# Optimization experiments

Hardware: AMD Instinct MI355X
Metric: run time of the kernel (lower is better)

Reference implementation:

```python
import jax, jax.numpy as jnp
import numpy as np

EPS = 1e-4  # BatchNorm2d eps from source


def binarize(x):
    # brevitas 1-bit quant: sign(x) with sign(0)=+1; straight-through (clipped) estimator
    y = jnp.clip(x, -1.0, 1.0)
    q = jnp.where(x >= 0, 1.0, -1.0).astype(x.dtype)
    return y + jax.lax.stop_gradient(q - y)


def bn(x, g, b, m, v):
    inv = g / jnp.sqrt(v + EPS)
    return x * inv[None, :, None, None] + (b - m * inv)[None, :, None, None]


def conv(x, w, pad):
    return jax.lax.conv_general_dilated(
        x, w, window_strides=(1, 1), padding=[(pad, pad), (pad, pad)],
        dimension_numbers=('NCHW', 'OIHW', 'NCHW'))


def conv_mod(x, w1, bn1, w3, bn3):
    # conv1x1(binary W) -> BN -> binarize act -> conv3x3(binary W) -> BN -> binarize act
    x = conv(x, binarize(w1), 0)
    x = binarize(bn(x, *bn1))
    x = conv(x, binarize(w3), 1)
    x = binarize(bn(x, *bn3))
    return x


def maxpool2(x):
    return jax.lax.reduce_window(x, -jnp.inf, jax.lax.max,
                                 (1, 1, 2, 2), (1, 1, 2, 2), 'VALID')


def setup_inputs() -> dict:
    key = jax.random.key(0)
    ks = jax.random.split(key, 24)
    B, Cin, down, up, H, W = 16, 256, 64, 256, 56, 56
    d = {
        'x':   jax.random.normal(ks[0], (B, Cin, H, W), jnp.float32),
        'w11': jax.random.normal(ks[1], (down, Cin, 1, 1), jnp.float32) * 0.1,
        'w31': jax.random.normal(ks[2], (up, down, 3, 3), jnp.float32) * 0.1,
        'w12': jax.random.normal(ks[3], (down, up, 1, 1), jnp.float32) * 0.1,
        'w32': jax.random.normal(ks[4], (up, down, 3, 3), jnp.float32) * 0.1,
    }
    # BatchNorm params (inference stats): gamma, beta, running mean, running var
    for i, (tag, c) in enumerate([('11', down), ('31', up), ('12', down), ('32', up)]):
        d['g' + tag] = jax.random.uniform(ks[5 + 4 * i], (c,), jnp.float32, 0.5, 1.5)
        d['b' + tag] = jax.random.normal(ks[6 + 4 * i], (c,), jnp.float32) * 0.1
        d['m' + tag] = jax.random.normal(ks[7 + 4 * i], (c,), jnp.float32) * 0.1
        d['v' + tag] = jax.random.uniform(ks[8 + 4 * i], (c,), jnp.float32, 0.5, 1.5)
    return d


def reference(x, w11, w31, w12, w32,
              g11, b11, m11, v11, g31, b31, m31, v31,
              g12, b12, m12, v12, g32, b32, m32, v32):
    h = conv_mod(x, w11, (g11, b11, m11, v11), w31, (g31, b31, m31, v31))
    r = conv_mod(h, w12, (g12, b12, m12, v12), w32, (g32, b32, m32, v32))
    s = binarize(h + r)          # quant_add: re-binarize the residual sum
    return maxpool2(s)           # MaxPool2d(2)
```

## Files before the change

### kernel.cpp

```cpp
#include <hip/hip_runtime.h>
#include <stdint.h>

#pragma clang fp contract(off)


#define HW_   3136
#define NPIX  50176

#define OFF_W31B   0
#define OFF_W12B   18432
#define OFF_W32B   20480
#define OFF_IV11   38912
#define OFF_IV31   39424
#define OFF_IV12   41472
#define OFF_IV32   41984
#define OFF_SGNT   44032
#define OFF_A1     109568
#define OFF_A2     510976
#define OFF_H      912384
#define OFF_S      2518016

__device__ inline float2 mk_ivbt(float g, float b, float m, float v) {
    float inv  = __fdiv_rn(g, __fsqrt_rn(__fadd_rn(v, 1e-4f)));
    float beta = __fsub_rn(b, __fmul_rn(m, inv));
    return make_float2(inv, beta);
}

__global__ __launch_bounds__(256) void k0_all(
    const float* __restrict__ w11, const float* __restrict__ w31,
    const float* __restrict__ w12, const float* __restrict__ w32,
    const float* __restrict__ g11, const float* __restrict__ b11,
    const float* __restrict__ m11, const float* __restrict__ v11,
    const float* __restrict__ g31, const float* __restrict__ b31,
    const float* __restrict__ m31, const float* __restrict__ v31,
    const float* __restrict__ g12, const float* __restrict__ b12,
    const float* __restrict__ m12, const float* __restrict__ v12,
    const float* __restrict__ g32, const float* __restrict__ b32,
    const float* __restrict__ m32, const float* __restrict__ v32,
    uint64_t* __restrict__ W31b, uint64_t* __restrict__ W12b,
    uint64_t* __restrict__ W32b,
    float2* __restrict__ iv11, float2* __restrict__ iv31,
    float2* __restrict__ iv12, float2* __restrict__ iv32,
    float* __restrict__ sgnT)
{
    int blk = blockIdx.x;
    if (blk < 1216) {
        int wid = blk * 4 + (threadIdx.x >> 6);
        int l = threadIdx.x & 63;
        if (wid < 2304) {
            int co = wid / 9, tap = wid % 9;
            uint64_t bits = __ballot(w31[(co * 64 + l) * 9 + tap] >= 0.f);
            if (l == 0) W31b[wid] = bits;
        } else if (wid < 4608) {
            int i = wid - 2304;
            int co = i / 9, tap = i % 9;
            uint64_t bits = __ballot(w32[(co * 64 + l) * 9 + tap] >= 0.f);
            if (l == 0) W32b[i] = bits;
        } else if (wid < 4864) {
            int i = wid - 4608;
            int co = i >> 2, k = i & 3;
            uint64_t bits = __ballot(w12[co * 256 + k * 64 + l] >= 0.f);
            if (l == 0) W12b[i] = bits;
        }
    } else if (blk < 1219) {
        int i = (blk - 1216) * 256 + threadIdx.x;
        if (i < 64)        iv11[i]       = mk_ivbt(g11[i],       b11[i],       m11[i],       v11[i]);
        else if (i < 320)  iv31[i - 64]  = mk_ivbt(g31[i - 64],  b31[i - 64],  m31[i - 64],  v31[i - 64]);
        else if (i < 384)  iv12[i - 320] = mk_ivbt(g12[i - 320], b12[i - 320], m12[i - 320], v12[i - 320]);
        else if (i < 640)  iv32[i - 384] = mk_ivbt(g32[i - 384], b32[i - 384], m32[i - 384], v32[i - 384]);
    } else {
        int t = (blk - 1219) * 256 + threadIdx.x;
        int j = t >> 8, ci = t & 255;
        sgnT[ci * 64 + j] = (w11[t] >= 0.f) ? 1.0f : -1.0f;
    }
}

__global__ __launch_bounds__(512) void k1_conv1(
    const float* __restrict__ x, const float* __restrict__ sgnT,
    const float2* __restrict__ ivbt, unsigned char* __restrict__ A1)
{
    __shared__ float sgn[16384];

#pragma unroll
    for (int i = 0; i < 32; ++i)
        sgn[i * 512 + threadIdx.x] = sgnT[i * 512 + threadIdx.x];

    const int l = threadIdx.x & 63;
    const int g = __builtin_amdgcn_readfirstlane(threadIdx.x >> 6);
    const int P = blockIdx.x * 128 + l * 2;
    const int bl = P / HW_;
    const int pxl = P - bl * HW_;
    const float* xp = x + (size_t)bl * (256 * HW_) + pxl;
    const float* sg = sgn + g * 8;

    float acc[8][2];
#pragma unroll
    for (int j = 0; j < 8; ++j) { acc[j][0] = 0.0f; acc[j][1] = 0.0f; }

    float2 b0[8], b1[8], b2[8], b3[8];

#define PF(B, CI0)                                                          \
    _Pragma("unroll")                                                       \
    for (int k = 0; k < 8; ++k)                                             \
        B[k] = *(const float2*)(xp + (size_t)((CI0) + k) * HW_);

#define COMP(B, CI0)                                                        \
    _Pragma("unroll")                                                       \
    for (int k = 0; k < 8; ++k) {                                           \
        const float* s_ = sg + ((CI0) + k) * 64;                            \
        _Pragma("unroll")                                                   \
        for (int j = 0; j < 8; ++j) {                                       \
            acc[j][0] = __builtin_fmaf(s_[j], B[k].x, acc[j][0]);           \
            acc[j][1] = __builtin_fmaf(s_[j], B[k].y, acc[j][1]);           \
        }                                                                   \
    }

    PF(b0, 0) PF(b1, 8) PF(b2, 16)

    __syncthreads();

    for (int cb = 0; cb < 256; cb += 32) {
        PF(b3, cb + 24) COMP(b0, cb)
        if (cb < 224) {
            PF(b0, cb + 32) COMP(b1, cb + 8)
            PF(b1, cb + 40) COMP(b2, cb + 16)
            PF(b2, cb + 48) COMP(b3, cb + 24)
        } else {
            COMP(b1, 232) COMP(b2, 240) COMP(b3, 248)
        }
    }
#undef PF
#undef COMP

    unsigned bp0 = 0, bp1 = 0;
#pragma unroll
    for (int j = 0; j < 8; ++j) {
        float2 ib = ivbt[g * 8 + j];
        bp0 |= (__fadd_rn(__fmul_rn(acc[j][0], ib.x), ib.y) >= 0.0f) ? (1u << j) : 0u;
        bp1 |= (__fadd_rn(__fmul_rn(acc[j][1], ib.x), ib.y) >= 0.0f) ? (1u << j) : 0u;
    }
    unsigned char* a = A1 + (size_t)P * 8 + g;
    a[0] = (unsigned char)bp0;
    a[8] = (unsigned char)bp1;
}

template <bool MERGE>
__global__ __launch_bounds__(256) void k_conv3b(
    const uint64_t* __restrict__ A, const uint64_t* __restrict__ Wb,
    const float2* __restrict__ ivbt, const uint64_t* __restrict__ Hin,
    uint64_t* __restrict__ Out)
{
    __shared__ uint64_t tile[4 * 58];
    const int l = threadIdx.x & 63;
    const int wv = threadIdx.x >> 6;
    const int chunk = blockIdx.x;
    const int b = chunk / 49;
    const int hw0 = (chunk % 49) * 64;
    const int r0 = hw0 / 56;
    const int o  = hw0 % 56;
    const int rfirst = r0 - 1;

    {
        int idx = threadIdx.x;
        if (idx < 4 * 58) {
            int rr = idx / 58, cc = idx % 58;
            int gh = rfirst + rr, gw = cc - 1;
            uint64_t v = 0;
            if ((unsigned)gh < 56u && (unsigned)gw < 56u)
                v = A[b * HW_ + gh * 56 + gw];
            tile[idx] = v;
        }
    }

    const int co = wv * 64 + l;
    uint64_t wp[9];
    int c64[9];
#pragma unroll
    for (int t = 0; t < 9; ++t) {
        wp[t] = Wb[co * 9 + t];
        c64[t] = 64 - 2 * (int)__popcll(wp[t]);
    }
    const float2 ib = ivbt[co];

    __syncthreads();

    uint64_t res = 0;
    for (int p = 0; p < 64; ++p) {
        const int inrow2 = (p >= 56 - o) ? 1 : 0;
        const int w = o + p - (inrow2 ? 56 : 0);
        const int row = r0 + inrow2;
        const int rbase = inrow2 * 58;

        int s = 0;
#pragma unroll
        for (int dr = 0; dr < 3; ++dr)
#pragma unroll
            for (int dc = 0; dc < 3; ++dc) {
                uint64_t a = tile[rbase + dr * 58 + w + dc];
                s += (int)__popcll(a ^ wp[dr * 3 + dc]);
            }
        int y = 576 - 2 * s;

        unsigned um = 0;
        if (row == 0)  um |= 0x007u;
        if (row == 55) um |= 0x1C0u;
        if (w == 0)    um |= 0x049u;
        if (w == 55)   um |= 0x124u;
        if (um) {
#pragma unroll
            for (int t = 0; t < 9; ++t)
                if ((um >> t) & 1u) y -= c64[t];
        }

        float val = __fadd_rn(__fmul_rn((float)y, ib.x), ib.y);
        uint64_t word = __ballot(val >= 0.0f);
        res = (l == p) ? word : res;
    }

    size_t oidx = (size_t)wv * NPIX + (size_t)(b * HW_) + hw0 + l;
    if (MERGE) res |= Hin[oidx];
    Out[oidx] = res;
}

__global__ __launch_bounds__(256) void k3_conv1b(
    const uint64_t* __restrict__ H, const uint64_t* __restrict__ W12b,
    const float2* __restrict__ ivbt, uint64_t* __restrict__ A2)
{
    int p = blockIdx.x * 256 + threadIdx.x;
    uint64_t h0 = H[p];
    uint64_t h1 = H[NPIX + p];
    uint64_t h2 = H[2 * NPIX + p];
    uint64_t h3 = H[3 * NPIX + p];
    uint64_t bits = 0;
#pragma unroll 4
    for (int co = 0; co < 64; ++co) {
        const uint64_t* wp = W12b + co * 4;
        int s = (int)(__popcll(h0 ^ wp[0]) + __popcll(h1 ^ wp[1]) +
                      __popcll(h2 ^ wp[2]) + __popcll(h3 ^ wp[3]));
        int y = 256 - 2 * s;
        float2 ib = ivbt[co];
        float val = __fadd_rn(__fmul_rn((float)y, ib.x), ib.y);
        bits |= (uint64_t)(val >= 0.0f) << co;
    }
    A2[p] = bits;
}

__global__ __launch_bounds__(256) void k4b_pool(
    const uint64_t* __restrict__ S, float* __restrict__ out)
{
    int o = blockIdx.x * 256 + threadIdx.x;
    int ow = o % 28;
    int t = o / 28;
    int oh = t % 28; t /= 28;
    int co = t & 255;
    int b  = t >> 8;
    int k = co >> 6, j = co & 63;
    const uint64_t* Sk = S + (size_t)k * NPIX + (size_t)(b * HW_) + (2 * oh) * 56 + 2 * ow;
    uint64_t s = Sk[0] | Sk[1] | Sk[56] | Sk[57];
    out[o] = ((s >> j) & 1) ? 1.0f : -1.0f;
}

extern "C" void kernel_launch(void* const* d_in, const int* in_sizes, int n_in,
                              void* d_out, int out_size, void* d_ws, size_t ws_size,
                              hipStream_t stream)
{
    const float* x   = (const float*)d_in[0];
    const float* w11 = (const float*)d_in[1];
    const float* w31 = (const float*)d_in[2];
    const float* w12 = (const float*)d_in[3];
    const float* w32 = (const float*)d_in[4];
    const float* g11 = (const float*)d_in[5];
    const float* b11 = (const float*)d_in[6];
    const float* m11 = (const float*)d_in[7];
    const float* v11 = (const float*)d_in[8];
    const float* g31 = (const float*)d_in[9];
    const float* b31 = (const float*)d_in[10];
    const float* m31 = (const float*)d_in[11];
    const float* v31 = (const float*)d_in[12];
    const float* g12 = (const float*)d_in[13];
    const float* b12 = (const float*)d_in[14];
    const float* m12 = (const float*)d_in[15];
    const float* v12 = (const float*)d_in[16];
    const float* g32 = (const float*)d_in[17];
    const float* b32 = (const float*)d_in[18];
    const float* m32 = (const float*)d_in[19];
    const float* v32 = (const float*)d_in[20];

    char* ws = (char*)d_ws;
    uint64_t* W31b = (uint64_t*)(ws + OFF_W31B);
    uint64_t* W12b = (uint64_t*)(ws + OFF_W12B);
    uint64_t* W32b = (uint64_t*)(ws + OFF_W32B);
    float2* iv11 = (float2*)(ws + OFF_IV11);
    float2* iv31 = (float2*)(ws + OFF_IV31);
    float2* iv12 = (float2*)(ws + OFF_IV12);
    float2* iv32 = (float2*)(ws + OFF_IV32);
    float*  sgnT = (float*)(ws + OFF_SGNT);
    uint64_t* A1 = (uint64_t*)(ws + OFF_A1);
    uint64_t* A2 = (uint64_t*)(ws + OFF_A2);
    uint64_t* Hb = (uint64_t*)(ws + OFF_H);
    uint64_t* Sb = (uint64_t*)(ws + OFF_S);

    k0_all<<<dim3(1283), dim3(256), 0, stream>>>(
        w11, w31, w12, w32,
        g11, b11, m11, v11, g31, b31, m31, v31,
        g12, b12, m12, v12, g32, b32, m32, v32,
        W31b, W12b, W32b, iv11, iv31, iv12, iv32, sgnT);

    k1_conv1<<<dim3(392), dim3(512), 0, stream>>>(x, sgnT, iv11, (unsigned char*)A1);

    k_conv3b<false><<<dim3(784), dim3(256), 0, stream>>>(A1, W31b, iv31, (const uint64_t*)nullptr, Hb);

    k3_conv1b<<<dim3(196), dim3(256), 0, stream>>>(Hb, W12b, iv12, A2);

    k_conv3b<true><<<dim3(784), dim3(256), 0, stream>>>(A2, W32b, iv32, Hb, Sb);

    k4b_pool<<<dim3(12544), dim3(256), 0, stream>>>(Sb, (float*)d_out);
}
```

Baseline: 125.8 us.

## Fuse binary 1x1 conv into first 3x3 conv; drop LDS sign staging in conv1

The separate k3_conv1b kernel is folded into the first k_conv3b launch. Each block shares its freshly computed H words through LDS, and each wave computes 16 of the 64 output channels, writing 16-bit fragments of A2. This removes a launch and a global read of H. Separately, k1_conv1 no longer copies the sign matrix into LDS and reads it directly from global memory. Its prefetch pipeline shrinks from four buffers to two and adds per-iteration barriers, which may lower memory-level parallelism in that kernel.

```diff
diff --git a/kernel.cpp b/kernel.cpp
--- a/kernel.cpp
+++ b/kernel.cpp
@@ -79,25 +79,19 @@
     const float* __restrict__ x, const float* __restrict__ sgnT,
     const float2* __restrict__ ivbt, unsigned char* __restrict__ A1)
 {
-    __shared__ float sgn[16384];
-
-#pragma unroll
-    for (int i = 0; i < 32; ++i)
-        sgn[i * 512 + threadIdx.x] = sgnT[i * 512 + threadIdx.x];
-
     const int l = threadIdx.x & 63;
     const int g = __builtin_amdgcn_readfirstlane(threadIdx.x >> 6);
     const int P = blockIdx.x * 128 + l * 2;
     const int bl = P / HW_;
     const int pxl = P - bl * HW_;
     const float* xp = x + (size_t)bl * (256 * HW_) + pxl;
-    const float* sg = sgn + g * 8;
+    const float* sg = sgnT + g * 8;
 
     float acc[8][2];
 #pragma unroll
     for (int j = 0; j < 8; ++j) { acc[j][0] = 0.0f; acc[j][1] = 0.0f; }
 
-    float2 b0[8], b1[8], b2[8], b3[8];
+    float2 bufA[8], bufB[8];
 
 #define PF(B, CI0)                                                          \
     _Pragma("unroll")                                                       \
@@ -115,19 +109,14 @@
         }                                                                   \
     }
 
-    PF(b0, 0) PF(b1, 8) PF(b2, 16)
-
-    __syncthreads();
-
-    for (int cb = 0; cb < 256; cb += 32) {
-        PF(b3, cb + 24) COMP(b0, cb)
-        if (cb < 224) {
-            PF(b0, cb + 32) COMP(b1, cb + 8)
-            PF(b1, cb + 40) COMP(b2, cb + 16)
-            PF(b2, cb + 48) COMP(b3, cb + 24)
-        } else {
-            COMP(b1, 232) COMP(b2, 240) COMP(b3, 248)
-        }
+    for (int cb = 0; cb < 256; cb += 16) {
+        __syncthreads();
+        if (cb == 0) { PF(bufA, 0) }
+        PF(bufB, cb + 8)
+        COMP(bufA, cb)
+        __syncthreads();
+        if (cb + 16 < 256) { PF(bufA, cb + 16) }
+        COMP(bufB, cb + 8)
     }
 #undef PF
 #undef COMP
@@ -144,13 +133,16 @@
     a[8] = (unsigned char)bp1;
 }
 
-template <bool MERGE>
+template <bool MERGE, bool DO_K3>
 __global__ __launch_bounds__(256) void k_conv3b(
     const uint64_t* __restrict__ A, const uint64_t* __restrict__ Wb,
     const float2* __restrict__ ivbt, const uint64_t* __restrict__ Hin,
-    uint64_t* __restrict__ Out)
+    uint64_t* __restrict__ Out,
+    const uint64_t* __restrict__ W12b, const float2* __restrict__ iv12,
+    unsigned short* __restrict__ A2)
 {
     __shared__ uint64_t tile[4 * 58];
+    __shared__ uint64_t sh4[4][64];
     const int l = threadIdx.x & 63;
     const int wv = threadIdx.x >> 6;
     const int chunk = blockIdx.x;
@@ -220,29 +212,25 @@
     size_t oidx = (size_t)wv * NPIX + (size_t)(b * HW_) + hw0 + l;
     if (MERGE) res |= Hin[oidx];
     Out[oidx] = res;
-}
-
-__global__ __launch_bounds__(256) void k3_conv1b(
-    const uint64_t* __restrict__ H, const uint64_t* __restrict__ W12b,
-    const float2* __restrict__ ivbt, uint64_t* __restrict__ A2)
-{
-    int p = blockIdx.x * 256 + threadIdx.x;
-    uint64_t h0 = H[p];
-    uint64_t h1 = H[NPIX + p];
-    uint64_t h2 = H[2 * NPIX + p];
-    uint64_t h3 = H[3 * NPIX + p];
-    uint64_t bits = 0;
-#pragma unroll 4
-    for (int co = 0; co < 64; ++co) {
-        const uint64_t* wp = W12b + co * 4;
-        int s = (int)(__popcll(h0 ^ wp[0]) + __popcll(h1 ^ wp[1]) +
-                      __popcll(h2 ^ wp[2]) + __popcll(h3 ^ wp[3]));
-        int y = 256 - 2 * s;
-        float2 ib = ivbt[co];
-        float val = __fadd_rn(__fmul_rn((float)y, ib.x), ib.y);
-        bits |= (uint64_t)(val >= 0.0f) << co;
-    }
-    A2[p] = bits;
+
+    if (DO_K3) {
+        sh4[wv][l] = res;
+        __syncthreads();
+        uint64_t h0 = sh4[0][l], h1 = sh4[1][l], h2 = sh4[2][l], h3 = sh4[3][l];
+        unsigned bits16 = 0;
+#pragma unroll
+        for (int jj = 0; jj < 16; ++jj) {
+            int cq = wv * 16 + jj;
+            const uint64_t* wq = W12b + cq * 4;
+            int s = (int)(__popcll(h0 ^ wq[0]) + __popcll(h1 ^ wq[1]) +
+                          __popcll(h2 ^ wq[2]) + __popcll(h3 ^ wq[3]));
+            int y = 256 - 2 * s;
+            float2 ibq = iv12[cq];
+            float val = __fadd_rn(__fmul_rn((float)y, ibq.x), ibq.y);
+            bits16 |= (val >= 0.0f) ? (1u << jj) : 0u;
+        }
+        A2[(size_t)(b * HW_ + hw0 + l) * 4 + wv] = (unsigned short)bits16;
+    }
 }
 
 __global__ __launch_bounds__(256) void k4b_pool(
@@ -308,11 +296,13 @@
 
     k1_conv1<<<dim3(392), dim3(512), 0, stream>>>(x, sgnT, iv11, (unsigned char*)A1);
 
-    k_conv3b<false><<<dim3(784), dim3(256), 0, stream>>>(A1, W31b, iv31, (const uint64_t*)nullptr, Hb);
-
-    k3_conv1b<<<dim3(196), dim3(256), 0, stream>>>(Hb, W12b, iv12, A2);
-
-    k_conv3b<true><<<dim3(784), dim3(256), 0, stream>>>(A2, W32b, iv32, Hb, Sb);
+    k_conv3b<false, true><<<dim3(784), dim3(256), 0, stream>>>(
+        A1, W31b, iv31, (const uint64_t*)nullptr, Hb,
+        W12b, iv12, (unsigned short*)A2);
+
+    k_conv3b<true, false><<<dim3(784), dim3(256), 0, stream>>>(
+        A2, W32b, iv32, Hb, Sb,
+        (const uint64_t*)nullptr, (const float2*)nullptr, (unsigned short*)nullptr);
 
     k4b_pool<<<dim3(12544), dim3(256), 0, stream>>>(Sb, (float*)d_out);
 }
```

Measured after the change: 119.8 us. 4.7% less time.
